# Performance work log

Hardware: AMD Instinct MI355X
Metric: run time of the kernel (lower is better)

## Reference

```python
import jax, jax.numpy as jnp
import numpy as np

B, N, D = 1, 4096, 3072
H, DH = 16, 64
INNER = H * DH  # 1024
SCALE = DH ** -0.5
EPS = 1e-5


def setup_inputs() -> dict:
    key = jax.random.key(0)
    ks = jax.random.split(key, 4)
    x = jax.random.normal(ks[0], (B, N, D), jnp.float32)
    pe = jax.random.normal(ks[1], (1, 1, N, DH // 2, 2, 2), jnp.float32)
    w_qkv = jax.random.normal(ks[2], (3 * INNER, D), jnp.float32) * 0.02
    w_out = jax.random.normal(ks[3], (D, INNER), jnp.float32) * 0.02
    ln_g = jnp.ones((D,), jnp.float32)
    ln_b = jnp.zeros((D,), jnp.float32)
    return {"x": x, "pe": pe, "w_qkv": w_qkv, "w_out": w_out, "ln_g": ln_g, "ln_b": ln_b}


def _apply_rope(t, pe):
    # t: [b,h,n,d], pe: [1,1,n,d/2,2,2] (Flux rope layout)
    b, h, n, d = t.shape
    t_ = t.reshape(b, h, n, d // 2, 1, 2)
    out = pe[..., 0] * t_[..., 0] + pe[..., 1] * t_[..., 1]  # [b,h,n,d/2,2]
    return out.reshape(b, h, n, d)


def reference(x, pe, w_qkv, w_out, ln_g, ln_b):
    # LayerNorm (norm2)
    mu = jnp.mean(x, axis=-1, keepdims=True)
    var = jnp.mean((x - mu) ** 2, axis=-1, keepdims=True)
    xn = (x - mu) / jnp.sqrt(var + EPS) * ln_g + ln_b
    # QKV projection (no bias)
    qkv = xn @ w_qkv.T  # [b,n,3*inner]
    q, k, v = jnp.split(qkv, 3, axis=-1)
    def split_heads(t):
        return t.reshape(B, N, H, DH).transpose(0, 2, 1, 3)  # b h n d
    q, k, v = split_heads(q), split_heads(k), split_heads(v)
    # RoPE on q and k (attention_aug_bbox with mask=None, aug idx = -1 -> plain rope attn)
    q = _apply_rope(q, pe)
    k = _apply_rope(k, pe)
    scores = jnp.einsum('bhqd,bhkd->bhqk', q, k) * SCALE
    attn = jax.nn.softmax(scores, axis=-1)
    o = jnp.einsum('bhqk,bhkd->bhqd', attn, v)
    o = o.transpose(0, 2, 1, 3).reshape(B, N, INNER)  # b n (h d)
    return o @ w_out.T  # [b,n,dim]
```

## Files before the change

kernel.cpp:

```cpp
#include <hip/hip_runtime.h>
#include <hip/hip_bf16.h>

typedef unsigned short u16;
typedef __attribute__((ext_vector_type(8))) short bf16x8;
typedef __attribute__((ext_vector_type(4))) float f32x4;

#define N_TOK 4096
#define DMODEL 3072
#define NH 16
#define DHEAD 64
#define INNER 1024
#define SCALE_LOG2E 0.18033688011112042f

__device__ __forceinline__ u16 f2bf(float f) {
    union { float f; unsigned u; } un; un.f = f;
    unsigned r = un.u + 0x7fffu + ((un.u >> 16) & 1u);
    return (u16)(r >> 16);
}
__device__ __forceinline__ float bf2f(u16 u) {
    union { unsigned u; float f; } x; x.u = ((unsigned)u) << 16; return x.f;
}
__device__ __forceinline__ unsigned pk2bf(float a, float b) {
    union { float f; unsigned u; } ua, ub; ua.f = a; ub.f = b;
    return __builtin_amdgcn_perm(ub.u + 0x8000u, ua.u + 0x8000u, 0x07060302u);
}
__device__ __forceinline__ void load_lds16(const u16* g, u16* l) {
    __builtin_amdgcn_global_load_lds(
        (const __attribute__((address_space(1))) unsigned int*)g,
        (__attribute__((address_space(3))) unsigned int*)l, 16, 0, 0);
}

__device__ __forceinline__ bf16x8 build_bp(unsigned u0, unsigned u1,
                                           unsigned w0, unsigned w1) {
    auto a = __builtin_amdgcn_permlane32_swap(u0, w0, false, false);
    auto b = __builtin_amdgcn_permlane16_swap(a[0], a[1], false, false);
    auto c = __builtin_amdgcn_permlane32_swap(u1, w1, false, false);
    auto d = __builtin_amdgcn_permlane16_swap(c[0], c[1], false, false);
    union { unsigned w[4]; bf16x8 v; } r;
    r.w[0] = b[0]; r.w[1] = d[0]; r.w[2] = b[1]; r.w[3] = d[1];
    return r.v;
}

__global__ __launch_bounds__(256) void prep(const float* __restrict__ x,
                                            const float* __restrict__ g,
                                            const float* __restrict__ b,
                                            u16* __restrict__ xn,
                                            const float* __restrict__ w_qkv,
                                            u16* __restrict__ wq,
                                            const float* __restrict__ w_out,
                                            u16* __restrict__ wo) {
    int bid = blockIdx.x;
    int tid = threadIdx.x;
    if (bid < 4096) {
        int row = bid;
        const float4* xr = (const float4*)(x + (size_t)row * DMODEL);
        float4 v[3];
        float s = 0.f, ss = 0.f;
#pragma unroll
        for (int i = 0; i < 3; ++i) {
            v[i] = xr[i * 256 + tid];
            s  += v[i].x + v[i].y + v[i].z + v[i].w;
            ss += v[i].x * v[i].x + v[i].y * v[i].y + v[i].z * v[i].z + v[i].w * v[i].w;
        }
#pragma unroll
        for (int off = 32; off; off >>= 1) {
            s  += __shfl_xor(s, off);
            ss += __shfl_xor(ss, off);
        }
        __shared__ float red[8];
        int wid = tid >> 6, lane = tid & 63;
        if (lane == 0) { red[wid] = s; red[wid + 4] = ss; }
        __syncthreads();
        s  = red[0] + red[1] + red[2] + red[3];
        ss = red[4] + red[5] + red[6] + red[7];
        float mean = s * (1.f / DMODEL);
        float var  = ss * (1.f / DMODEL) - mean * mean;
        float rstd = rsqrtf(var + 1e-5f);
        ushort4* orow = (ushort4*)(xn + (size_t)row * DMODEL);
#pragma unroll
        for (int i = 0; i < 3; ++i) {
            float4 gg = ((const float4*)g)[i * 256 + tid];
            float4 bb = ((const float4*)b)[i * 256 + tid];
            ushort4 o;
            o.x = f2bf((v[i].x - mean) * rstd * gg.x + bb.x);
            o.y = f2bf((v[i].y - mean) * rstd * gg.y + bb.y);
            o.z = f2bf((v[i].z - mean) * rstd * gg.z + bb.z);
            o.w = f2bf((v[i].w - mean) * rstd * gg.w + bb.w);
            orow[i * 256 + tid] = o;
        }
    } else if (bid < 4096 + 2048) {
        const int n4 = 3 * INNER * DMODEL / 4;
        for (int i = (bid - 4096) * 256 + tid; i < n4; i += 2048 * 256) {
            float4 v = ((const float4*)w_qkv)[i];
            ushort4 o;
            o.x = f2bf(v.x); o.y = f2bf(v.y); o.z = f2bf(v.z); o.w = f2bf(v.w);
            ((ushort4*)wq)[i] = o;
        }
    } else {
        const int n4 = DMODEL * INNER / 4;
        for (int i = (bid - 6144) * 256 + tid; i < n4; i += 512 * 256) {
            float4 v = ((const float4*)w_out)[i];
            ushort4 o;
            o.x = f2bf(v.x); o.y = f2bf(v.y); o.z = f2bf(v.z); o.w = f2bf(v.w);
            ((ushort4*)wo)[i] = o;
        }
    }
}


#define VM5 asm volatile("s_waitcnt vmcnt(5)" ::: "memory")
#define VM4 asm volatile("s_waitcnt vmcnt(4)" ::: "memory")
#define VM3 asm volatile("s_waitcnt vmcnt(3)" ::: "memory")
#define VM0 asm volatile("s_waitcnt vmcnt(0)" ::: "memory")
#define LGK8 asm volatile("s_waitcnt lgkmcnt(8)" ::: "memory")
#define NOPS ((void)0)

#define ST_A(d, h, t) do { \
    load_lds16(pA##h##0 + (size_t)(t) * 64, &lds[(d) * 16384 + (h) * 8192 + dq]); \
    load_lds16(pA##h##1 + (size_t)(t) * 64, &lds[(d) * 16384 + (h) * 8192 + dq + 512]); \
  } while (0)
#define ST_B1(d, u, t) \
    load_lds16(pB##u + (size_t)(t) * 64, &lds[32768 + (d) * 12288 + (u) * 4096 + wid * 512])

#define PHASE(d, p, STAGE, PRE, POST) do { \
    bf16x8 afr[2][2]; \
    if ((p) == 0) { \
      _Pragma("unroll") for (int nf = 0; nf < 3; ++nf) { \
        bfr[nf][0] = *(const bf16x8*)&lds[32768 + (d) * 12288 + baseB + nf * 1024 + c0]; \
        bfr[nf][1] = *(const bf16x8*)&lds[32768 + (d) * 12288 + baseB + nf * 1024 + c1]; \
      } \
    } \
    _Pragma("unroll") for (int mfl = 0; mfl < 2; ++mfl) { \
      afr[mfl][0] = *(const bf16x8*)&lds[(d) * 16384 + (p) * 4096 + mfl * 1024 + baseA + c0]; \
      afr[mfl][1] = *(const bf16x8*)&lds[(d) * 16384 + (p) * 4096 + mfl * 1024 + baseA + c1]; \
    } \
    STAGE; \
    PRE; \
    __builtin_amdgcn_s_barrier(); \
    asm volatile("s_waitcnt lgkmcnt(0)" ::: "memory"); \
    __builtin_amdgcn_sched_barrier(0); \
    __builtin_amdgcn_s_setprio(1); \
    _Pragma("unroll") for (int mfl = 0; mfl < 2; ++mfl) \
      _Pragma("unroll") for (int nf = 0; nf < 3; ++nf) { \
        acc[(p) * 2 + mfl][nf] = __builtin_amdgcn_mfma_f32_16x16x32_bf16(afr[mfl][0], bfr[nf][0], acc[(p) * 2 + mfl][nf], 0, 0, 0); \
        acc[(p) * 2 + mfl][nf] = __builtin_amdgcn_mfma_f32_16x16x32_bf16(afr[mfl][1], bfr[nf][1], acc[(p) * 2 + mfl][nf], 0, 0, 0); \
      } \
    __builtin_amdgcn_s_setprio(0); \
    POST; \
    __builtin_amdgcn_s_barrier(); \
  } while (0)

template <int MODE>
__global__ __launch_bounds__(512, 2) void gemm256(const u16* __restrict__ A,
                                                  const u16* __restrict__ B,
                                                  void* __restrict__ C,
                                                  int M, int Nn, int K,
                                                  const float* __restrict__ pe,
                                                  u16* __restrict__ Qr,
                                                  u16* __restrict__ Kr,
                                                  u16* __restrict__ Vt) {
    __shared__ u16 lds[57344];
    const int tid = threadIdx.x;
    const int lane = tid & 63, wid = tid >> 6;
    const int wm = wid >> 2, wn = wid & 3;
    const int l15 = lane & 15, quad = lane >> 4;
    const int sw = l15 & 7;

    int nbx = Nn / 192;
    int cpx = gridDim.x >> 3;
    int wg = (blockIdx.x & 7) * cpx + (blockIdx.x >> 3);
    int m0 = (wg / nbx) << 8, n0 = (wg % nbx) * 192;

    const int baseA = wm * 2048 + l15 * 64;
    const int baseB = wn * 3072 + l15 * 64;
    const int c0 = (quad ^ sw) * 8;
    const int c1 = ((4 + quad) ^ sw) * 8;
    const int dq = wid * 1024;

    const u16 *pA00, *pA01, *pA10, *pA11, *pB0, *pB1, *pB2;
    {
        int scol = ((lane & 7) ^ (lane >> 3)) * 8;
#define MKSRCA(h, j, PA) { \
        int ell = (h) * 128 + (wid * 2 + (j)) * 8 + (lane >> 3); \
        int g = ell >> 6, wmh = (ell >> 5) & 1, r = ell & 31; \
        PA = A + (size_t)(m0 + wmh * 128 + g * 32 + r) * K + scol; }
#define MKSRCB(u, PB) { \
        int ell = (u) * 64 + wid * 8 + (lane >> 3); \
        PB = B + (size_t)(n0 + ell) * K + scol; }
        MKSRCA(0, 0, pA00) MKSRCA(0, 1, pA01)
        MKSRCA(1, 0, pA10) MKSRCA(1, 1, pA11)
        MKSRCB(0, pB0) MKSRCB(1, pB1) MKSRCB(2, pB2)
#undef MKSRCA
#undef MKSRCB
    }

    f32x4 acc[8][3];
    f32x4 zero4 = {0.f, 0.f, 0.f, 0.f};
#pragma unroll
    for (int i = 0; i < 8; ++i)
#pragma unroll
        for (int j = 0; j < 3; ++j) acc[i][j] = zero4;
    bf16x8 bfr[3][2];

    ST_B1(0, 0, 0); ST_B1(0, 1, 0); ST_B1(0, 2, 0); ST_A(0, 0, 0); ST_A(0, 1, 0);
    ST_B1(1, 0, 1); ST_B1(1, 1, 1); ST_B1(1, 2, 1); ST_A(1, 0, 1);
    VM5;
    __builtin_amdgcn_s_barrier();

    const int NIT = (K >> 7) - 1;
    for (int i = 0; i < NIT; ++i) {
        int t = 2 * i;
        PHASE(0, 0, ST_A(1, 1, t + 1), LGK8, NOPS);
        PHASE(0, 1, ST_B1(0, 0, t + 2), NOPS, NOPS);
        PHASE(0, 2, ST_B1(0, 1, t + 2), NOPS, NOPS);
        PHASE(0, 3, ST_B1(0, 2, t + 2), NOPS, VM3);
        PHASE(1, 0, ST_A(0, 0, t + 2), LGK8, NOPS);
        PHASE(1, 1, ST_A(0, 1, t + 2), NOPS, NOPS);
        PHASE(1, 2, ST_B1(1, 0, t + 3), NOPS, NOPS);
        PHASE(1, 3, { ST_B1(1, 1, t + 3); ST_B1(1, 2, t + 3); ST_A(1, 0, t + 3); }, NOPS, VM5);
    }
    {
        int T = K >> 6;
        PHASE(0, 0, ST_A(1, 1, T - 1), LGK8, NOPS);
        PHASE(0, 1, NOPS, NOPS, NOPS);
        PHASE(0, 2, NOPS, NOPS, NOPS);
        PHASE(0, 3, NOPS, NOPS, VM0);
        PHASE(1, 0, NOPS, LGK8, NOPS);
        PHASE(1, 1, NOPS, NOPS, NOPS);
        PHASE(1, 2, NOPS, NOPS, NOPS);
        PHASE(1, 3, NOPS, NOPS, NOPS);
    }

    if (MODE == 0) {
#pragma unroll
        for (int mf = 0; mf < 8; ++mf)
#pragma unroll
            for (int nf = 0; nf < 3; ++nf)
#pragma unroll
                for (int r = 0; r < 4; ++r) {
                    int rr = m0 + wm * 128 + mf * 16 + quad * 4 + r;
                    int cc = n0 + wn * 48 + nf * 16 + l15;
                    ((float*)C)[(size_t)rr * Nn + cc] = acc[mf][nf][r];
                }
    } else {
#pragma unroll
        for (int nf = 0; nf < 3; ++nf) {
            int cc = n0 + wn * 48 + nf * 16 + l15;
            if (cc < 2048) {
                const int isQ = (cc < 1024);
                const float scl = isQ ? SCALE_LOG2E : 1.f;
                u16* dst = isQ ? Qr : Kr;
                int hh = (cc & 1023) >> 6;
                int ii = (cc & 63) >> 1;
                int jj = cc & 1;
#pragma unroll
                for (int mf = 0; mf < 8; ++mf)
#pragma unroll
                    for (int r = 0; r < 4; ++r) {
                        int rr = m0 + wm * 128 + mf * 16 + quad * 4 + r;
                        float v = acc[mf][nf][r];
                        float vp = __shfl_xor(v, 1);
                        float v0 = jj ? vp : v;
                        float v1 = jj ? v : vp;
                        const float* pw = pe + (size_t)rr * 128 + ii * 4 + jj * 2;
                        float ov = (pw[0] * v0 + pw[1] * v1) * scl;
                        dst[((size_t)hh * N_TOK + rr) * 64 + (cc & 63)] = f2bf(ov);
                    }
            } else {
                int hh = (cc - 2048) >> 6, dd = cc & 63;
#pragma unroll
                for (int mf = 0; mf < 8; ++mf) {
                    int rr = m0 + wm * 128 + mf * 16 + quad * 4;
                    ushort4 o4;
                    o4.x = f2bf(acc[mf][nf][0]); o4.y = f2bf(acc[mf][nf][1]);
                    o4.z = f2bf(acc[mf][nf][2]); o4.w = f2bf(acc[mf][nf][3]);
                    *(ushort4*)&Vt[((size_t)hh * 64 + dd) * N_TOK + rr] = o4;
                }
            }
        }
    }
}


#define FA_STAGE3(dst, kt) do { \
    load_lds16(&Kh[(size_t)((kt) + krow) * DHEAD + csw], &lds_all[(dst) + kbase]); \
    load_lds16(&Kh[(size_t)((kt) + krow + 8) * DHEAD + csw], &lds_all[(dst) + kbase + 512]); \
    load_lds16(&Vh[(size_t)krow * N_TOK + (kt) + csw], &lds_all[(dst) + 4096 + kbase]); \
    load_lds16(&Vh[(size_t)(krow + 8) * N_TOK + (kt) + csw], &lds_all[(dst) + 4096 + kbase + 512]); \
  } while (0)

__global__ __launch_bounds__(256, 2) void flash_attn(const u16* __restrict__ Q,
                                                     const u16* __restrict__ K,
                                                     const u16* __restrict__ Vt,
                                                     u16* __restrict__ O) {
    __shared__ u16 lds_all[24576];
    int tid = threadIdx.x, lane = tid & 63, wid = tid >> 6;
    int l15 = lane & 15, quad = lane >> 4;
    int sw = l15 & 7;
    int h = blockIdx.y;
    int q0 = blockIdx.x * 128 + wid * 32;
    const u16* Qh = Q + (size_t)h * N_TOK * DHEAD;
    const u16* Kh = K + (size_t)h * N_TOK * DHEAD;
    const u16* Vh = Vt + (size_t)h * DHEAD * N_TOK;

    f32x4 zero4 = {0.f, 0.f, 0.f, 0.f};
    bf16x8 ones;
#pragma unroll
    for (int i = 0; i < 8; ++i) ones[i] = (short)0x3F80;

    bf16x8 aq[2][2];
#pragma unroll
    for (int mtQ = 0; mtQ < 2; ++mtQ)
#pragma unroll
        for (int kc = 0; kc < 2; ++kc)
            aq[mtQ][kc] = *(const bf16x8*)&Qh[(size_t)(q0 + mtQ * 16 + l15) * DHEAD + kc * 32 + quad * 8];

    f32x4 o[2][4], lacc[2];
#pragma unroll
    for (int mtQ = 0; mtQ < 2; ++mtQ) {
#pragma unroll
        for (int dt = 0; dt < 4; ++dt) o[mtQ][dt] = zero4;
        lacc[mtQ] = zero4;
    }

    int rowoff = lane >> 3;
    int krow = wid * 16 + rowoff;
    int kbase = wid * 1024;
    int csw = ((lane & 7) ^ rowoff) * 8;

    FA_STAGE3(0, 0);
    FA_STAGE3(8192, 64);
    VM4;
    __builtin_amdgcn_s_barrier();
    __builtin_amdgcn_sched_barrier(0);

    int cur = 0;
    for (int t = 0; t < 64; ++t) {
        int stg = cur + 16384; if (stg >= 24576) stg -= 24576;
        bf16x8 bk[4][2], av[4][2];
#pragma unroll
        for (int tt = 0; tt < 4; ++tt)
#pragma unroll
            for (int kc = 0; kc < 2; ++kc)
                bk[tt][kc] = *(const bf16x8*)&lds_all[cur + (tt * 16 + l15) * 64 + (((kc * 4 + quad) ^ sw) * 8)];
        __builtin_amdgcn_sched_barrier(0);
#pragma unroll
        for (int tt = 0; tt < 4; ++tt)
#pragma unroll
            for (int kc = 0; kc < 2; ++kc)
                av[tt][kc] = *(const bf16x8*)&lds_all[cur + 4096 + (tt * 16 + l15) * 64 + (((kc * 4 + quad) ^ sw) * 8)];
        __builtin_amdgcn_sched_barrier(0);
        if (t < 62) FA_STAGE3(stg, (t + 2) * 64);
        asm volatile("s_waitcnt lgkmcnt(8)" ::: "memory");
        __builtin_amdgcn_sched_barrier(0);

        bf16x8 bp[2][2];
#pragma unroll
        for (int mtQ = 0; mtQ < 2; ++mtQ) {
            f32x4 s[4];
            __builtin_amdgcn_s_setprio(1);
#pragma unroll
            for (int ntK = 0; ntK < 4; ++ntK) {
                f32x4 t0 = __builtin_amdgcn_mfma_f32_16x16x32_bf16(bk[ntK][0], aq[mtQ][0], zero4, 0, 0, 0);
                s[ntK] = __builtin_amdgcn_mfma_f32_16x16x32_bf16(bk[ntK][1], aq[mtQ][1], t0, 0, 0, 0);
            }
            __builtin_amdgcn_s_setprio(0);
            unsigned pw[4][2];
#pragma unroll
            for (int ntK = 0; ntK < 4; ++ntK) {
                pw[ntK][0] = pk2bf(__builtin_amdgcn_exp2f(s[ntK][0]), __builtin_amdgcn_exp2f(s[ntK][1]));
                pw[ntK][1] = pk2bf(__builtin_amdgcn_exp2f(s[ntK][2]), __builtin_amdgcn_exp2f(s[ntK][3]));
            }
            bp[mtQ][0] = build_bp(pw[0][0], pw[0][1], pw[1][0], pw[1][1]);
            bp[mtQ][1] = build_bp(pw[2][0], pw[2][1], pw[3][0], pw[3][1]);
        }

        asm volatile("s_waitcnt lgkmcnt(0)" ::: "memory");
        __builtin_amdgcn_sched_barrier(0);
        __builtin_amdgcn_s_setprio(1);
#pragma unroll
        for (int mtQ = 0; mtQ < 2; ++mtQ) {
            lacc[mtQ] = __builtin_amdgcn_mfma_f32_16x16x32_bf16(ones, bp[mtQ][0], lacc[mtQ], 0, 0, 0);
            lacc[mtQ] = __builtin_amdgcn_mfma_f32_16x16x32_bf16(ones, bp[mtQ][1], lacc[mtQ], 0, 0, 0);
#pragma unroll
            for (int dt = 0; dt < 4; ++dt) {
                o[mtQ][dt] = __builtin_amdgcn_mfma_f32_16x16x32_bf16(av[dt][0], bp[mtQ][0], o[mtQ][dt], 0, 0, 0);
                o[mtQ][dt] = __builtin_amdgcn_mfma_f32_16x16x32_bf16(av[dt][1], bp[mtQ][1], o[mtQ][dt], 0, 0, 0);
            }
        }
        __builtin_amdgcn_s_setprio(0);

        if (t < 62) { VM4; } else if (t == 62) { VM0; }
        __builtin_amdgcn_s_barrier();
        __builtin_amdgcn_sched_barrier(0);
        cur += 8192; if (cur >= 24576) cur -= 24576;
    }

    __syncthreads();
    u16* scratch = lds_all + wid * 2048;
#pragma unroll
    for (int mtQ = 0; mtQ < 2; ++mtQ) {
        float rl = 1.f / lacc[mtQ][0];
#pragma unroll
        for (int dt = 0; dt < 4; ++dt) {
            uint2 ov;
            ov.x = pk2bf(o[mtQ][dt][0] * rl, o[mtQ][dt][1] * rl);
            ov.y = pk2bf(o[mtQ][dt][2] * rl, o[mtQ][dt][3] * rl);
            *(uint2*)&scratch[(mtQ * 16 + l15) * 64 + dt * 16 + quad * 4] = ov;
        }
    }
    __syncthreads();
#pragma unroll
    for (int p = 0; p < 4; ++p) {
        int q_local = p * 8 + (lane >> 3);
        int dcol = (lane & 7) * 8;
        bf16x8 v = *(const bf16x8*)&scratch[q_local * 64 + dcol];
        *(bf16x8*)&O[(size_t)(q0 + q_local) * INNER + h * 64 + dcol] = v;
    }
}

extern "C" void kernel_launch(void* const* d_in, const int* in_sizes, int n_in,
                              void* d_out, int out_size, void* d_ws, size_t ws_size,
                              hipStream_t stream) {
    const float* x     = (const float*)d_in[0];
    const float* pe    = (const float*)d_in[1];
    const float* w_qkv = (const float*)d_in[2];
    const float* w_out = (const float*)d_in[3];
    const float* ln_g  = (const float*)d_in[4];
    const float* ln_b  = (const float*)d_in[5];
    float* out = (float*)d_out;

    char* ws = (char*)d_ws;
    u16* xn  = (u16*)ws;  ws += (size_t)N_TOK * DMODEL * 2;
    u16* wq  = (u16*)ws;  ws += (size_t)3 * INNER * DMODEL * 2;
    u16* wo  = (u16*)ws;  ws += (size_t)DMODEL * INNER * 2;
    u16* Qr  = (u16*)ws;  ws += (size_t)NH * N_TOK * DHEAD * 2;
    u16* Kr  = (u16*)ws;  ws += (size_t)NH * N_TOK * DHEAD * 2;
    u16* Vt  = (u16*)ws;  ws += (size_t)NH * DHEAD * N_TOK * 2;
    u16* Ob  = (u16*)ws;  ws += (size_t)N_TOK * INNER * 2;

    prep<<<4096 + 2048 + 512, 256, 0, stream>>>(x, ln_g, ln_b, xn, w_qkv, wq, w_out, wo);
    gemm256<2><<<dim3((N_TOK / 256) * (DMODEL / 192)), 512, 0, stream>>>(
        xn, wq, nullptr, N_TOK, DMODEL, DMODEL, pe, Qr, Kr, Vt);
    flash_attn<<<dim3(N_TOK / 128, NH), 256, 0, stream>>>(Qr, Kr, Vt, Ob);
    gemm256<0><<<dim3((N_TOK / 256) * (DMODEL / 192)), 512, 0, stream>>>(
        Ob, wo, out, N_TOK, DMODEL, INNER, nullptr, nullptr, nullptr, nullptr);
}
```

Measured before the change: 348.9 us.

## Software-pipeline flash attention: overlap next tile QK^T with current softmax/PV

Restructures the flash attention main loop into a two-stage software pipeline with ping-pong score and V register buffers. Each iteration computes QK^T for tile t+1 while doing the exp, pack and PV MFMAs for tile t, so the matrix-core work can hide transcendental latency. It also replaces the manual bf16 pack with the hardware v_cvt_pk_bf16_f32 instruction. The cost is more live registers per thread, which could cause spills or lower occupancy at launch_bounds(256,2), and a manually unrolled prologue and epilogue.

```diff
diff --git a/kernel.cpp b/kernel.cpp
--- a/kernel.cpp
+++ b/kernel.cpp
@@ -289,6 +289,54 @@
     load_lds16(&Vh[(size_t)(krow + 8) * N_TOK + (kt) + csw], &lds_all[(dst) + 4096 + kbase + 512]); \
   } while (0)
 
+#define FA_READ(CUR, AV) do { \
+    _Pragma("unroll") for (int tt = 0; tt < 4; ++tt) \
+      _Pragma("unroll") for (int kc = 0; kc < 2; ++kc) \
+        bk[tt][kc] = *(const bf16x8*)&lds_all[(CUR) + (tt * 16 + l15) * 64 + (((kc * 4 + quad) ^ sw) * 8)]; \
+    __builtin_amdgcn_sched_barrier(0); \
+    _Pragma("unroll") for (int tt = 0; tt < 4; ++tt) \
+      _Pragma("unroll") for (int kc = 0; kc < 2; ++kc) \
+        AV[tt][kc] = *(const bf16x8*)&lds_all[(CUR) + 4096 + (tt * 16 + l15) * 64 + (((kc * 4 + quad) ^ sw) * 8)]; \
+    __builtin_amdgcn_sched_barrier(0); \
+  } while (0)
+
+#define LGK8F do { asm volatile("s_waitcnt lgkmcnt(8)" ::: "memory"); __builtin_amdgcn_sched_barrier(0); } while (0)
+#define LGK0F do { asm volatile("s_waitcnt lgkmcnt(0)" ::: "memory"); __builtin_amdgcn_sched_barrier(0); } while (0)
+
+#define FA_QK(S) do { \
+    __builtin_amdgcn_s_setprio(1); \
+    _Pragma("unroll") for (int mtQ = 0; mtQ < 2; ++mtQ) \
+      _Pragma("unroll") for (int ntK = 0; ntK < 4; ++ntK) { \
+        f32x4 t0 = __builtin_amdgcn_mfma_f32_16x16x32_bf16(bk[ntK][0], aq[mtQ][0], zero4, 0, 0, 0); \
+        S[mtQ][ntK] = __builtin_amdgcn_mfma_f32_16x16x32_bf16(bk[ntK][1], aq[mtQ][1], t0, 0, 0, 0); \
+      } \
+    __builtin_amdgcn_s_setprio(0); \
+  } while (0)
+
+#define FA_SMPV(SP, AVP) do { \
+    _Pragma("unroll") for (int mtQ = 0; mtQ < 2; ++mtQ) { \
+      unsigned pw[4][2]; \
+      _Pragma("unroll") for (int ntK = 0; ntK < 4; ++ntK) { \
+        float e0 = __builtin_amdgcn_exp2f(SP[mtQ][ntK][0]); \
+        float e1 = __builtin_amdgcn_exp2f(SP[mtQ][ntK][1]); \
+        float e2 = __builtin_amdgcn_exp2f(SP[mtQ][ntK][2]); \
+        float e3 = __builtin_amdgcn_exp2f(SP[mtQ][ntK][3]); \
+        asm("v_cvt_pk_bf16_f32 %0, %1, %2" : "=v"(pw[ntK][0]) : "v"(e0), "v"(e1)); \
+        asm("v_cvt_pk_bf16_f32 %0, %1, %2" : "=v"(pw[ntK][1]) : "v"(e2), "v"(e3)); \
+      } \
+      bf16x8 bp0 = build_bp(pw[0][0], pw[0][1], pw[1][0], pw[1][1]); \
+      bf16x8 bp1 = build_bp(pw[2][0], pw[2][1], pw[3][0], pw[3][1]); \
+      __builtin_amdgcn_s_setprio(1); \
+      lacc[mtQ] = __builtin_amdgcn_mfma_f32_16x16x32_bf16(ones, bp0, lacc[mtQ], 0, 0, 0); \
+      lacc[mtQ] = __builtin_amdgcn_mfma_f32_16x16x32_bf16(ones, bp1, lacc[mtQ], 0, 0, 0); \
+      _Pragma("unroll") for (int dt = 0; dt < 4; ++dt) { \
+        o[mtQ][dt] = __builtin_amdgcn_mfma_f32_16x16x32_bf16(AVP[dt][0], bp0, o[mtQ][dt], 0, 0, 0); \
+        o[mtQ][dt] = __builtin_amdgcn_mfma_f32_16x16x32_bf16(AVP[dt][1], bp1, o[mtQ][dt], 0, 0, 0); \
+      } \
+      __builtin_amdgcn_s_setprio(0); \
+    } \
+  } while (0)
+
 __global__ __launch_bounds__(256, 2) void flash_attn(const u16* __restrict__ Q,
                                                      const u16* __restrict__ K,
                                                      const u16* __restrict__ Vt,
@@ -328,73 +376,56 @@
     int kbase = wid * 1024;
     int csw = ((lane & 7) ^ rowoff) * 8;
 
+    bf16x8 bk[4][2], avA[4][2], avB[4][2];
+    f32x4 sA[2][4], sB[2][4];
+
     FA_STAGE3(0, 0);
     FA_STAGE3(8192, 64);
     VM4;
     __builtin_amdgcn_s_barrier();
     __builtin_amdgcn_sched_barrier(0);
 
-    int cur = 0;
-    for (int t = 0; t < 64; ++t) {
-        int stg = cur + 16384; if (stg >= 24576) stg -= 24576;
-        bf16x8 bk[4][2], av[4][2];
-#pragma unroll
-        for (int tt = 0; tt < 4; ++tt)
-#pragma unroll
-            for (int kc = 0; kc < 2; ++kc)
-                bk[tt][kc] = *(const bf16x8*)&lds_all[cur + (tt * 16 + l15) * 64 + (((kc * 4 + quad) ^ sw) * 8)];
-        __builtin_amdgcn_sched_barrier(0);
-#pragma unroll
-        for (int tt = 0; tt < 4; ++tt)
-#pragma unroll
-            for (int kc = 0; kc < 2; ++kc)
-                av[tt][kc] = *(const bf16x8*)&lds_all[cur + 4096 + (tt * 16 + l15) * 64 + (((kc * 4 + quad) ^ sw) * 8)];
-        __builtin_amdgcn_sched_barrier(0);
-        if (t < 62) FA_STAGE3(stg, (t + 2) * 64);
-        asm volatile("s_waitcnt lgkmcnt(8)" ::: "memory");
-        __builtin_amdgcn_sched_barrier(0);
-
-        bf16x8 bp[2][2];
-#pragma unroll
-        for (int mtQ = 0; mtQ < 2; ++mtQ) {
-            f32x4 s[4];
-            __builtin_amdgcn_s_setprio(1);
-#pragma unroll
-            for (int ntK = 0; ntK < 4; ++ntK) {
-                f32x4 t0 = __builtin_amdgcn_mfma_f32_16x16x32_bf16(bk[ntK][0], aq[mtQ][0], zero4, 0, 0, 0);
-                s[ntK] = __builtin_amdgcn_mfma_f32_16x16x32_bf16(bk[ntK][1], aq[mtQ][1], t0, 0, 0, 0);
-            }
-            __builtin_amdgcn_s_setprio(0);
-            unsigned pw[4][2];
-#pragma unroll
-            for (int ntK = 0; ntK < 4; ++ntK) {
-                pw[ntK][0] = pk2bf(__builtin_amdgcn_exp2f(s[ntK][0]), __builtin_amdgcn_exp2f(s[ntK][1]));
-                pw[ntK][1] = pk2bf(__builtin_amdgcn_exp2f(s[ntK][2]), __builtin_amdgcn_exp2f(s[ntK][3]));
-            }
-            bp[mtQ][0] = build_bp(pw[0][0], pw[0][1], pw[1][0], pw[1][1]);
-            bp[mtQ][1] = build_bp(pw[2][0], pw[2][1], pw[3][0], pw[3][1]);
-        }
-
-        asm volatile("s_waitcnt lgkmcnt(0)" ::: "memory");
-        __builtin_amdgcn_sched_barrier(0);
-        __builtin_amdgcn_s_setprio(1);
-#pragma unroll
-        for (int mtQ = 0; mtQ < 2; ++mtQ) {
-            lacc[mtQ] = __builtin_amdgcn_mfma_f32_16x16x32_bf16(ones, bp[mtQ][0], lacc[mtQ], 0, 0, 0);
-            lacc[mtQ] = __builtin_amdgcn_mfma_f32_16x16x32_bf16(ones, bp[mtQ][1], lacc[mtQ], 0, 0, 0);
-#pragma unroll
-            for (int dt = 0; dt < 4; ++dt) {
-                o[mtQ][dt] = __builtin_amdgcn_mfma_f32_16x16x32_bf16(av[dt][0], bp[mtQ][0], o[mtQ][dt], 0, 0, 0);
-                o[mtQ][dt] = __builtin_amdgcn_mfma_f32_16x16x32_bf16(av[dt][1], bp[mtQ][1], o[mtQ][dt], 0, 0, 0);
-            }
-        }
-        __builtin_amdgcn_s_setprio(0);
-
-        if (t < 62) { VM4; } else if (t == 62) { VM0; }
+    FA_READ(0, avA);
+    FA_STAGE3(16384, 128);
+    LGK8F;
+    FA_QK(sA);
+    LGK0F;
+    VM4;
+    __builtin_amdgcn_s_barrier();
+    __builtin_amdgcn_sched_barrier(0);
+
+    int cur = 8192;
+    for (int i = 0; i < 31; ++i) {
+        int tB = 2 * i + 1, tA = 2 * i + 2;
+        FA_READ(cur, avB);
+        { int stg = cur + 16384; if (stg >= 24576) stg -= 24576;
+          FA_STAGE3(stg, (tB + 2) * 64); }
+        LGK8F;
+        FA_QK(sB);
+        FA_SMPV(sA, avA);
+        LGK0F;
+        VM4;
         __builtin_amdgcn_s_barrier();
         __builtin_amdgcn_sched_barrier(0);
         cur += 8192; if (cur >= 24576) cur -= 24576;
-    }
+        FA_READ(cur, avA);
+        if (tA + 2 < 64) { int stg = cur + 16384; if (stg >= 24576) stg -= 24576;
+                           FA_STAGE3(stg, (tA + 2) * 64); }
+        LGK8F;
+        FA_QK(sA);
+        FA_SMPV(sB, avB);
+        LGK0F;
+        if (tA + 2 < 64) { VM4; } else { VM0; }
+        __builtin_amdgcn_s_barrier();
+        __builtin_amdgcn_sched_barrier(0);
+        cur += 8192; if (cur >= 24576) cur -= 24576;
+    }
+    FA_READ(cur, avB);
+    LGK8F;
+    FA_QK(sB);
+    FA_SMPV(sA, avA);
+    LGK0F;
+    FA_SMPV(sB, avB);
 
     __syncthreads();
     u16* scratch = lds_all + wid * 2048;
```

New measurement: 331.1 us. -5.1%, faster.
